# Performance work log

Hardware: AMD Instinct MI355X
Metric: run time of the kernel (lower is better)

Reference implementation:

```python
import jax, jax.numpy as jnp
import numpy as np
import math

B, C, L, N, HEAD, M, DEPTH = 16, 256, 64, 8192, 8, 12, 1
PI = math.pi
MODES = jnp.arange(M, dtype=jnp.float32) / M  # modes_list = i/num_basis


def conv1d(x, w, b=None):
    # 1x1 Conv1d == channel matmul. x: (B,Cin,T), w: (Cout,Cin)
    y = jnp.einsum('oc,bcn->bon', w, x)
    if b is not None:
        y = y + b[None, :, None]
    return y


def split_heads(x):
    # (B,C,T) -> (B,H,T,c)  matching view(B,head,C//head,T).permute(0,1,3,2)
    b, c, t = x.shape
    return x.reshape(b, HEAD, c // HEAD, t).transpose(0, 1, 3, 2)


def merge_heads(x):
    # (B,H,T,c) -> (B,C,T)
    b, h, t, c = x.shape
    return x.transpose(0, 1, 3, 2).reshape(b, h * c, t)


def self_attn(q, k, v):
    # NOTE: source multiplies by dim**0.5 (not 1/sqrt(dim)); keep faithful.
    dim = q.shape[-1]
    a = jax.nn.softmax(jnp.einsum('bhlc,bhsc->bhls', q, k) * (dim ** 0.5), axis=-1)
    return jnp.einsum('bhls,bhsc->bhlc', a, v)


def encoder(x, enc_w, enc_b, weights):
    b, c, l = x.shape
    qkv = conv1d(x, enc_w, enc_b).reshape(b, 3, c, l)
    q = split_heads(qkv[:, 0])
    k = split_heads(qkv[:, 1])
    v = split_heads(qkv[:, 2])
    attn = merge_heads(self_attn(q, k, v))  # (B,C,L)
    # Fourier basis: cat(sin, cos) over num_basis modes -> (B,C,L,2M)
    ph = MODES[None, None, None, :] * attn[..., None] * PI
    basis = jnp.concatenate([jnp.sin(ph), jnp.cos(ph)], axis=-1)
    return jnp.einsum('bclm,cm->bcl', basis, weights) + x


def decoder(x, attn, dec_w, dec_b):
    kv = split_heads(attn)                      # (B,H,L,c) latent keys/values
    q = split_heads(conv1d(x, dec_w, dec_b))    # (B,H,N,c) point queries
    return merge_heads(self_attn(q, kv, kv)) + x


def bn_lrelu(x, g, b):
    # eval-mode BatchNorm1d (running_mean=0, running_var=1, eps=1e-5) + LeakyReLU(0.2)
    y = g[None, :, None] * x / jnp.sqrt(1.0 + 1e-5) + b[None, :, None]
    return jnp.where(y >= 0, y, 0.2 * y)


def setup_inputs() -> dict:
    key = jax.random.key(0)
    ks = jax.random.split(key, 8)
    return {
        'xt': jax.random.normal(ks[0], (B, C, L), jnp.float32),
        'xn': jax.random.normal(ks[1], (B, C, N), jnp.float32),
        'weights': jax.random.uniform(ks[2], (C, 2 * M), jnp.float32) / C,
        'mask_token': jax.random.normal(ks[3], (1, C, 1), jnp.float32) * 0.02,
        'enc_w': jax.random.normal(ks[4], (3 * C, C), jnp.float32) * 0.02,
        'enc_b': jnp.zeros((3 * C,), jnp.float32),
        'dec_w': jax.random.normal(ks[5], (C, C), jnp.float32) * 0.02,
        'dec_b': jnp.zeros((C,), jnp.float32),
        'fc1_w': jax.random.normal(ks[6], (C, C), jnp.float32) * 0.02,
        'fc1_g': jnp.ones((C,), jnp.float32),
        'fc1_b': jnp.zeros((C,), jnp.float32),
        'fc2_w': jax.random.normal(ks[7], (3, C), jnp.float32) * 0.02,
        'fc2_g': jnp.ones((3,), jnp.float32),
        'fc2_b': jnp.zeros((3,), jnp.float32),
    }


def reference(xt, xn, weights, mask_token, enc_w, enc_b, dec_w, dec_b,
              fc1_w, fc1_g, fc1_b, fc2_w, fc2_g, fc2_b):
    b = xt.shape[0]
    n = xn.shape[-1]
    # ratio=1.0 -> len_keep=0 -> fully masked: mask_token broadcast, under no_grad
    x_masked = jax.lax.stop_gradient(jnp.broadcast_to(mask_token, (b, C, n)))
    enc = xt
    x = x_masked
    for _ in range(DEPTH):
        enc = encoder(enc, enc_w, enc_b, weights)
        x = decoder(x, enc, dec_w, dec_b)
    xn_pre = x
    y = bn_lrelu(conv1d(xn_pre, fc1_w), fc1_g, fc1_b)
    y = bn_lrelu(conv1d(y, fc2_w), fc2_g, fc2_b)  # (B,3,N)
    return xn_pre, y.transpose(0, 2, 1)  # ((B,C,N), (B,N,3))
```

## Files before the change

kernel.cpp:

```cpp
#include <hip/hip_runtime.h>
#include <hip/hip_bf16.h>
#include <math.h>

#define B_    16
#define C_    256
#define L_    64
#define N_    8192
#define HEAD_ 8
#define HC_   32
#define M_    12

#define SQRT32F 5.656854249492380f
#define PI_F    3.14159265358979323846f
#define BN_INV  0.99999500003749969f

typedef float v4f __attribute__((ext_vector_type(4)));

__global__ __launch_bounds__(512) void enc_half(
    const float* __restrict__ xt, const float* __restrict__ enc_w,
    const float* __restrict__ enc_b, const float* __restrict__ weights,
    float* __restrict__ enc)
{
    __shared__ float Xs[C_][L_];
    __shared__ float qkv_s[96][68];
    __shared__ float P[32][68];
    __shared__ float wts[HC_][24];
    const int t    = threadIdx.x;
    const int b    = blockIdx.x >> 4;
    const int h    = (blockIdx.x >> 1) & 7;
    const int half = blockIdx.x & 1;
    const float* xtb = xt + (size_t)b * (C_ * L_);

    #pragma unroll
    for (int i = 0; i < 8; ++i) {
        int q = t + i * 512;
        int c = q >> 4, l4 = (q & 15) * 4;
        *reinterpret_cast<float4*>(&Xs[c][l4]) =
            *reinterpret_cast<const float4*>(&xtb[q * 4]);
    }
    #pragma unroll
    for (int idx = t; idx < HC_ * 24; idx += 512)
        wts[idx / 24][idx % 24] = weights[(h * HC_) * 24 + idx];
    __syncthreads();

    {
        const int kvr  = t >> 4;
        const int kvc4 = (t & 15) * 4;
        const int qr   = t >> 3;
        const int qc4  = half * 32 + (t & 7) * 4;
        const float* wk = enc_w + (size_t)(C_ + h * HC_ + kvr) * C_;
        const float* wv = enc_w + (size_t)(2 * C_ + h * HC_ + kvr) * C_;
        const float* wq = enc_w + (size_t)(h * HC_ + (qr & 31)) * C_;
        float4 acck = {}, accv = {}, accq = {};
        #pragma unroll 2
        for (int c0 = 0; c0 < C_; c0 += 4) {
            float4 xk0 = *reinterpret_cast<const float4*>(&Xs[c0 + 0][kvc4]);
            float4 xk1 = *reinterpret_cast<const float4*>(&Xs[c0 + 1][kvc4]);
            float4 xk2 = *reinterpret_cast<const float4*>(&Xs[c0 + 2][kvc4]);
            float4 xk3 = *reinterpret_cast<const float4*>(&Xs[c0 + 3][kvc4]);
            float4 wk4 = *reinterpret_cast<const float4*>(&wk[c0]);
            float4 wv4 = *reinterpret_cast<const float4*>(&wv[c0]);
            acck.x += wk4.x * xk0.x + wk4.y * xk1.x + wk4.z * xk2.x + wk4.w * xk3.x;
            acck.y += wk4.x * xk0.y + wk4.y * xk1.y + wk4.z * xk2.y + wk4.w * xk3.y;
            acck.z += wk4.x * xk0.z + wk4.y * xk1.z + wk4.z * xk2.z + wk4.w * xk3.z;
            acck.w += wk4.x * xk0.w + wk4.y * xk1.w + wk4.z * xk2.w + wk4.w * xk3.w;
            accv.x += wv4.x * xk0.x + wv4.y * xk1.x + wv4.z * xk2.x + wv4.w * xk3.x;
            accv.y += wv4.x * xk0.y + wv4.y * xk1.y + wv4.z * xk2.y + wv4.w * xk3.y;
            accv.z += wv4.x * xk0.z + wv4.y * xk1.z + wv4.z * xk2.z + wv4.w * xk3.z;
            accv.w += wv4.x * xk0.w + wv4.y * xk1.w + wv4.z * xk2.w + wv4.w * xk3.w;
            if (t < 256) {
                float4 xq0 = *reinterpret_cast<const float4*>(&Xs[c0 + 0][qc4]);
                float4 xq1 = *reinterpret_cast<const float4*>(&Xs[c0 + 1][qc4]);
                float4 xq2 = *reinterpret_cast<const float4*>(&Xs[c0 + 2][qc4]);
                float4 xq3 = *reinterpret_cast<const float4*>(&Xs[c0 + 3][qc4]);
                float4 wq4 = *reinterpret_cast<const float4*>(&wq[c0]);
                accq.x += wq4.x * xq0.x + wq4.y * xq1.x + wq4.z * xq2.x + wq4.w * xq3.x;
                accq.y += wq4.x * xq0.y + wq4.y * xq1.y + wq4.z * xq2.y + wq4.w * xq3.y;
                accq.z += wq4.x * xq0.z + wq4.y * xq1.z + wq4.z * xq2.z + wq4.w * xq3.z;
                accq.w += wq4.x * xq0.w + wq4.y * xq1.w + wq4.z * xq2.w + wq4.w * xq3.w;
            }
        }
        float bk = enc_b[C_ + h * HC_ + kvr];
        float bv = enc_b[2 * C_ + h * HC_ + kvr];
        acck.x += bk; acck.y += bk; acck.z += bk; acck.w += bk;
        accv.x += bv; accv.y += bv; accv.z += bv; accv.w += bv;
        *reinterpret_cast<float4*>(&qkv_s[32 + kvr][kvc4]) = acck;
        *reinterpret_cast<float4*>(&qkv_s[64 + kvr][kvc4]) = accv;
        if (t < 256) {
            float bq = enc_b[h * HC_ + qr];
            accq.x += bq; accq.y += bq; accq.z += bq; accq.w += bq;
            *reinterpret_cast<float4*>(&qkv_s[qr][qc4]) = accq;
        }
    }
    __syncthreads();

    {
        const int l   = t >> 4;
        const int lp0 = (t & 15) * 4;
        const int qcol = half * 32 + l;
        float4 a4 = {0.f, 0.f, 0.f, 0.f};
        #pragma unroll
        for (int cc = 0; cc < HC_; ++cc) {
            float qv_ = qkv_s[cc][qcol];
            float4 k4 = *reinterpret_cast<const float4*>(&qkv_s[32 + cc][lp0]);
            a4.x += qv_ * k4.x; a4.y += qv_ * k4.y;
            a4.z += qv_ * k4.z; a4.w += qv_ * k4.w;
        }
        a4.x *= SQRT32F; a4.y *= SQRT32F; a4.z *= SQRT32F; a4.w *= SQRT32F;
        *reinterpret_cast<float4*>(&P[l][lp0]) = a4;
    }
    __syncthreads();

    {
        int l = t >> 4, p0 = (t & 15) * 4;
        float m = -1e30f;
        #pragma unroll
        for (int j = 0; j < 4; ++j) m = fmaxf(m, P[l][p0 + j]);
        m = fmaxf(m, __shfl_xor(m, 1));
        m = fmaxf(m, __shfl_xor(m, 2));
        m = fmaxf(m, __shfl_xor(m, 4));
        m = fmaxf(m, __shfl_xor(m, 8));
        float sum = 0.f;
        #pragma unroll
        for (int j = 0; j < 4; ++j) {
            float e = __expf(P[l][p0 + j] - m);
            P[l][p0 + j] = e;
            sum += e;
        }
        sum += __shfl_xor(sum, 1);
        sum += __shfl_xor(sum, 2);
        sum += __shfl_xor(sum, 4);
        sum += __shfl_xor(sum, 8);
        float inv = 1.0f / sum;
        #pragma unroll
        for (int j = 0; j < 4; ++j) P[l][p0 + j] *= inv;
    }
    __syncthreads();

    {
        const int l0 = (t & 15) * 2;
        const int cc = t >> 4;
        float a0 = 0.f, a1 = 0.f;
        #pragma unroll
        for (int sq = 0; sq < 16; ++sq) {
            float4 p0v = *reinterpret_cast<const float4*>(&P[l0 + 0][sq * 4]);
            float4 p1v = *reinterpret_cast<const float4*>(&P[l0 + 1][sq * 4]);
            float4 v4  = *reinterpret_cast<const float4*>(&qkv_s[64 + cc][sq * 4]);
            a0 += p0v.x * v4.x + p0v.y * v4.y + p0v.z * v4.z + p0v.w * v4.w;
            a1 += p1v.x * v4.x + p1v.y * v4.y + p1v.z * v4.z + p1v.w * v4.w;
        }
        const float* wrf = wts[cc];
        const int c  = h * HC_ + cc;
        const int lg = half * 32 + l0;
        float av[2] = {a0, a1};
        float vv[2];
        #pragma unroll
        for (int i = 0; i < 2; ++i) {
            float val = Xs[c][lg + i] + wrf[M_];
            float base = av[i] * (PI_F / (float)M_);
            float s1, c1;
            __sincosf(base, &s1, &c1);
            float sm = 0.f, cm = 1.f;
            #pragma unroll
            for (int m = 1; m < M_; ++m) {
                float sp = sm * c1 + cm * s1;
                float cp = cm * c1 - sm * s1;
                sm = sp; cm = cp;
                val += wrf[m] * sm + wrf[M_ + m] * cm;
            }
            vv[i] = val;
        }
        *reinterpret_cast<float2*>(&enc[((size_t)b * C_ + c) * L_ + lg]) =
            make_float2(vv[0], vv[1]);
    }
}

__global__ __launch_bounds__(64) void dec_attn(const float* __restrict__ enc,
                                               const float* __restrict__ dec_w,
                                               const float* __restrict__ dec_b,
                                               const float* __restrict__ mt,
                                               float* __restrict__ xnp_out) {
    __shared__ float qvs[HC_];
    __shared__ float aw[L_];
    const int l = threadIdx.x;
    const int b = blockIdx.x >> 3;
    const int h = blockIdx.x & 7;
    const float* ench = enc + ((size_t)b * C_ + h * HC_) * L_;

    {
        int r = l >> 1, part = l & 1;
        const float* wr = dec_w + (size_t)(h * HC_ + r) * C_ + part * 128;
        const float* mp = mt + part * 128;
        float s = 0.f;
        #pragma unroll
        for (int j = 0; j < 32; ++j) {
            float4 w4 = *reinterpret_cast<const float4*>(&wr[j * 4]);
            float4 m4 = *reinterpret_cast<const float4*>(&mp[j * 4]);
            s += w4.x * m4.x + w4.y * m4.y + w4.z * m4.z + w4.w * m4.w;
        }
        s += __shfl_xor(s, 1);
        if (part == 0) qvs[r] = s + dec_b[h * HC_ + r];
    }
    __syncthreads();

    float s = 0.f;
    #pragma unroll
    for (int cc = 0; cc < HC_; ++cc)
        s += qvs[cc] * ench[cc * L_ + l];
    s *= SQRT32F;
    float m = s;
    #pragma unroll
    for (int off = 32; off >= 1; off >>= 1) m = fmaxf(m, __shfl_xor(m, off));
    float e = __expf(s - m);
    float sum = e;
    #pragma unroll
    for (int off = 32; off >= 1; off >>= 1) sum += __shfl_xor(sum, off);
    aw[l] = e / sum;
    __syncthreads();

    if (l < HC_) {
        const float* vrow = ench + l * L_;
        float a = 0.f;
        #pragma unroll
        for (int k4 = 0; k4 < L_; k4 += 4) {
            float4 a4 = *reinterpret_cast<const float4*>(&aw[k4]);
            float4 v4 = *reinterpret_cast<const float4*>(&vrow[k4]);
            a += a4.x * v4.x + a4.y * v4.y + a4.z * v4.z + a4.w * v4.w;
        }
        int c = h * HC_ + l;
        xnp_out[b * C_ + c] = a + mt[c];
    }
}

__global__ __launch_bounds__(256) void bcast_fc(const float* __restrict__ xnp,
                                                const float* __restrict__ fc1_w,
                                                const float* __restrict__ fc1_g,
                                                const float* __restrict__ fc1_b,
                                                const float* __restrict__ fc2_w,
                                                const float* __restrict__ fc2_g,
                                                const float* __restrict__ fc2_b,
                                                float* __restrict__ out) {
    const int t = threadIdx.x;
    const int blk = blockIdx.x;
    if (blk >= 16) {
        int rowid = blk - 16;
        float v = xnp[rowid];
        v4f V = {v, v, v, v};
        v4f* row = reinterpret_cast<v4f*>(out + (size_t)rowid * N_);
        #pragma unroll
        for (int i = 0; i < 8; ++i)
            __builtin_nontemporal_store(V, &row[t + i * 256]);
    } else {
        int b = blk;
        __shared__ float xs[C_];
        __shared__ float y1[C_];
        __shared__ float y2s[4];
        xs[t] = xnp[b * C_ + t];
        __syncthreads();
        {
            const float* wrow = fc1_w + (size_t)t * C_;
            float s = 0.f;
            #pragma unroll 8
            for (int c4 = 0; c4 < C_; c4 += 4) {
                float4 w4 = *reinterpret_cast<const float4*>(&wrow[c4]);
                float4 x4 = *reinterpret_cast<const float4*>(&xs[c4]);
                s += w4.x * x4.x + w4.y * x4.y + w4.z * x4.z + w4.w * x4.w;
            }
            float y = fc1_g[t] * s * BN_INV + fc1_b[t];
            y1[t] = (y >= 0.f) ? y : 0.2f * y;
        }
        __syncthreads();
        if (t < 3) {
            const float* wrow = fc2_w + t * C_;
            float s = 0.f;
            #pragma unroll 8
            for (int c4 = 0; c4 < C_; c4 += 4) {
                float4 w4 = *reinterpret_cast<const float4*>(&wrow[c4]);
                float4 x4 = *reinterpret_cast<const float4*>(&y1[c4]);
                s += w4.x * x4.x + w4.y * x4.y + w4.z * x4.z + w4.w * x4.w;
            }
            float y = fc2_g[t] * s * BN_INV + fc2_b[t];
            y2s[t] = (y >= 0.f) ? y : 0.2f * y;
        }
        __syncthreads();
        float v0 = y2s[0], v1 = y2s[1], v2 = y2s[2];
        v4f pat0 = {v0, v1, v2, v0};
        v4f pat1 = {v1, v2, v0, v1};
        v4f pat2 = {v2, v0, v1, v2};
        int r = t % 3;
        v4f a = (r == 0) ? pat0 : (r == 1) ? pat1 : pat2;
        v4f bb = (r == 0) ? pat1 : (r == 1) ? pat2 : pat0;
        v4f c = (r == 0) ? pat2 : (r == 1) ? pat0 : pat1;
        v4f* o1 = reinterpret_cast<v4f*>(
            out + (size_t)B_ * C_ * N_ + (size_t)b * (N_ * 3));
        #pragma unroll
        for (int i = 0; i < 24; i += 3) {
            __builtin_nontemporal_store(a,  &o1[t + (i + 0) * 256]);
            __builtin_nontemporal_store(bb, &o1[t + (i + 1) * 256]);
            __builtin_nontemporal_store(c,  &o1[t + (i + 2) * 256]);
        }
    }
}

extern "C" void kernel_launch(void* const* d_in, const int* in_sizes, int n_in,
                              void* d_out, int out_size, void* d_ws, size_t ws_size,
                              hipStream_t stream) {
    const float* xt      = (const float*)d_in[0];
    const float* weights = (const float*)d_in[2];
    const float* mt      = (const float*)d_in[3];
    const float* enc_w   = (const float*)d_in[4];
    const float* enc_b   = (const float*)d_in[5];
    const float* dec_w   = (const float*)d_in[6];
    const float* dec_b   = (const float*)d_in[7];
    const float* fc1_w   = (const float*)d_in[8];
    const float* fc1_g   = (const float*)d_in[9];
    const float* fc1_b   = (const float*)d_in[10];
    const float* fc2_w   = (const float*)d_in[11];
    const float* fc2_g   = (const float*)d_in[12];
    const float* fc2_b   = (const float*)d_in[13];

    float* ws  = (float*)d_ws;
    float* enc = ws;
    float* xnp = ws + 262144;

    float* out = (float*)d_out;

    enc_half<<<256, 512, 0, stream>>>(xt, enc_w, enc_b, weights, enc);
    dec_attn<<<128, 64, 0, stream>>>(enc, dec_w, dec_b, mt, xnp);
    bcast_fc<<<4112, 256, 0, stream>>>(xnp, fc1_w, fc1_g, fc1_b,
                                       fc2_w, fc2_g, fc2_b, out);
}
```

Measured before the change: 55.88 us.

## Fuse encoder, decoder, and broadcast kernels into one cooperative kernel

Merges the three kernels into a single cooperative launch of 256 blocks of 512 threads, separating the encoder, decoder-attention, and broadcast/FC phases with grid-wide syncs. The broadcast of 4096 rows is redistributed so that 240 blocks write 17 rows each and the first 16 blocks write one row each and also run the FC head. This removes two kernel launch gaps, at the cost of grid-barrier overhead and far fewer blocks issuing the large output stores (256 instead of 4112).

```diff
diff --git a/kernel.cpp b/kernel.cpp
--- a/kernel.cpp
+++ b/kernel.cpp
@@ -1,6 +1,9 @@
 #include <hip/hip_runtime.h>
+#include <hip/hip_cooperative_groups.h>
 #include <hip/hip_bf16.h>
 #include <math.h>
+
+namespace cg = cooperative_groups;
 
 #define B_    16
 #define C_    256
@@ -16,258 +19,268 @@
 
 typedef float v4f __attribute__((ext_vector_type(4)));
 
-__global__ __launch_bounds__(512) void enc_half(
+__global__ __launch_bounds__(512) void mega(
     const float* __restrict__ xt, const float* __restrict__ enc_w,
     const float* __restrict__ enc_b, const float* __restrict__ weights,
-    float* __restrict__ enc)
+    const float* __restrict__ dec_w, const float* __restrict__ dec_b,
+    const float* __restrict__ mt, const float* __restrict__ fc1_w,
+    const float* __restrict__ fc1_g, const float* __restrict__ fc1_b,
+    const float* __restrict__ fc2_w, const float* __restrict__ fc2_g,
+    const float* __restrict__ fc2_b, float* __restrict__ enc_g,
+    float* __restrict__ xnp_g, float* __restrict__ out)
 {
     __shared__ float Xs[C_][L_];
     __shared__ float qkv_s[96][68];
     __shared__ float P[32][68];
     __shared__ float wts[HC_][24];
-    const int t    = threadIdx.x;
-    const int b    = blockIdx.x >> 4;
-    const int h    = (blockIdx.x >> 1) & 7;
-    const int half = blockIdx.x & 1;
-    const float* xtb = xt + (size_t)b * (C_ * L_);
-
-    #pragma unroll
-    for (int i = 0; i < 8; ++i) {
-        int q = t + i * 512;
-        int c = q >> 4, l4 = (q & 15) * 4;
-        *reinterpret_cast<float4*>(&Xs[c][l4]) =
-            *reinterpret_cast<const float4*>(&xtb[q * 4]);
-    }
-    #pragma unroll
-    for (int idx = t; idx < HC_ * 24; idx += 512)
-        wts[idx / 24][idx % 24] = weights[(h * HC_) * 24 + idx];
-    __syncthreads();
-
-    {
-        const int kvr  = t >> 4;
-        const int kvc4 = (t & 15) * 4;
-        const int qr   = t >> 3;
-        const int qc4  = half * 32 + (t & 7) * 4;
-        const float* wk = enc_w + (size_t)(C_ + h * HC_ + kvr) * C_;
-        const float* wv = enc_w + (size_t)(2 * C_ + h * HC_ + kvr) * C_;
-        const float* wq = enc_w + (size_t)(h * HC_ + (qr & 31)) * C_;
-        float4 acck = {}, accv = {}, accq = {};
-        #pragma unroll 2
-        for (int c0 = 0; c0 < C_; c0 += 4) {
-            float4 xk0 = *reinterpret_cast<const float4*>(&Xs[c0 + 0][kvc4]);
-            float4 xk1 = *reinterpret_cast<const float4*>(&Xs[c0 + 1][kvc4]);
-            float4 xk2 = *reinterpret_cast<const float4*>(&Xs[c0 + 2][kvc4]);
-            float4 xk3 = *reinterpret_cast<const float4*>(&Xs[c0 + 3][kvc4]);
-            float4 wk4 = *reinterpret_cast<const float4*>(&wk[c0]);
-            float4 wv4 = *reinterpret_cast<const float4*>(&wv[c0]);
-            acck.x += wk4.x * xk0.x + wk4.y * xk1.x + wk4.z * xk2.x + wk4.w * xk3.x;
-            acck.y += wk4.x * xk0.y + wk4.y * xk1.y + wk4.z * xk2.y + wk4.w * xk3.y;
-            acck.z += wk4.x * xk0.z + wk4.y * xk1.z + wk4.z * xk2.z + wk4.w * xk3.z;
-            acck.w += wk4.x * xk0.w + wk4.y * xk1.w + wk4.z * xk2.w + wk4.w * xk3.w;
-            accv.x += wv4.x * xk0.x + wv4.y * xk1.x + wv4.z * xk2.x + wv4.w * xk3.x;
-            accv.y += wv4.x * xk0.y + wv4.y * xk1.y + wv4.z * xk2.y + wv4.w * xk3.y;
-            accv.z += wv4.x * xk0.z + wv4.y * xk1.z + wv4.z * xk2.z + wv4.w * xk3.z;
-            accv.w += wv4.x * xk0.w + wv4.y * xk1.w + wv4.z * xk2.w + wv4.w * xk3.w;
-            if (t < 256) {
-                float4 xq0 = *reinterpret_cast<const float4*>(&Xs[c0 + 0][qc4]);
-                float4 xq1 = *reinterpret_cast<const float4*>(&Xs[c0 + 1][qc4]);
-                float4 xq2 = *reinterpret_cast<const float4*>(&Xs[c0 + 2][qc4]);
-                float4 xq3 = *reinterpret_cast<const float4*>(&Xs[c0 + 3][qc4]);
-                float4 wq4 = *reinterpret_cast<const float4*>(&wq[c0]);
-                accq.x += wq4.x * xq0.x + wq4.y * xq1.x + wq4.z * xq2.x + wq4.w * xq3.x;
-                accq.y += wq4.x * xq0.y + wq4.y * xq1.y + wq4.z * xq2.y + wq4.w * xq3.y;
-                accq.z += wq4.x * xq0.z + wq4.y * xq1.z + wq4.z * xq2.z + wq4.w * xq3.z;
-                accq.w += wq4.x * xq0.w + wq4.y * xq1.w + wq4.z * xq2.w + wq4.w * xq3.w;
-            }
-        }
-        float bk = enc_b[C_ + h * HC_ + kvr];
-        float bv = enc_b[2 * C_ + h * HC_ + kvr];
-        acck.x += bk; acck.y += bk; acck.z += bk; acck.w += bk;
-        accv.x += bv; accv.y += bv; accv.z += bv; accv.w += bv;
-        *reinterpret_cast<float4*>(&qkv_s[32 + kvr][kvc4]) = acck;
-        *reinterpret_cast<float4*>(&qkv_s[64 + kvr][kvc4]) = accv;
-        if (t < 256) {
-            float bq = enc_b[h * HC_ + qr];
-            accq.x += bq; accq.y += bq; accq.z += bq; accq.w += bq;
-            *reinterpret_cast<float4*>(&qkv_s[qr][qc4]) = accq;
-        }
-    }
-    __syncthreads();
-
-    {
-        const int l   = t >> 4;
-        const int lp0 = (t & 15) * 4;
-        const int qcol = half * 32 + l;
-        float4 a4 = {0.f, 0.f, 0.f, 0.f};
-        #pragma unroll
-        for (int cc = 0; cc < HC_; ++cc) {
-            float qv_ = qkv_s[cc][qcol];
-            float4 k4 = *reinterpret_cast<const float4*>(&qkv_s[32 + cc][lp0]);
-            a4.x += qv_ * k4.x; a4.y += qv_ * k4.y;
-            a4.z += qv_ * k4.z; a4.w += qv_ * k4.w;
-        }
-        a4.x *= SQRT32F; a4.y *= SQRT32F; a4.z *= SQRT32F; a4.w *= SQRT32F;
-        *reinterpret_cast<float4*>(&P[l][lp0]) = a4;
-    }
-    __syncthreads();
-
-    {
-        int l = t >> 4, p0 = (t & 15) * 4;
-        float m = -1e30f;
-        #pragma unroll
-        for (int j = 0; j < 4; ++j) m = fmaxf(m, P[l][p0 + j]);
-        m = fmaxf(m, __shfl_xor(m, 1));
-        m = fmaxf(m, __shfl_xor(m, 2));
-        m = fmaxf(m, __shfl_xor(m, 4));
-        m = fmaxf(m, __shfl_xor(m, 8));
-        float sum = 0.f;
-        #pragma unroll
-        for (int j = 0; j < 4; ++j) {
-            float e = __expf(P[l][p0 + j] - m);
-            P[l][p0 + j] = e;
-            sum += e;
-        }
-        sum += __shfl_xor(sum, 1);
-        sum += __shfl_xor(sum, 2);
-        sum += __shfl_xor(sum, 4);
-        sum += __shfl_xor(sum, 8);
-        float inv = 1.0f / sum;
-        #pragma unroll
-        for (int j = 0; j < 4; ++j) P[l][p0 + j] *= inv;
-    }
-    __syncthreads();
-
-    {
-        const int l0 = (t & 15) * 2;
-        const int cc = t >> 4;
-        float a0 = 0.f, a1 = 0.f;
-        #pragma unroll
-        for (int sq = 0; sq < 16; ++sq) {
-            float4 p0v = *reinterpret_cast<const float4*>(&P[l0 + 0][sq * 4]);
-            float4 p1v = *reinterpret_cast<const float4*>(&P[l0 + 1][sq * 4]);
-            float4 v4  = *reinterpret_cast<const float4*>(&qkv_s[64 + cc][sq * 4]);
-            a0 += p0v.x * v4.x + p0v.y * v4.y + p0v.z * v4.z + p0v.w * v4.w;
-            a1 += p1v.x * v4.x + p1v.y * v4.y + p1v.z * v4.z + p1v.w * v4.w;
-        }
-        const float* wrf = wts[cc];
-        const int c  = h * HC_ + cc;
-        const int lg = half * 32 + l0;
-        float av[2] = {a0, a1};
-        float vv[2];
-        #pragma unroll
-        for (int i = 0; i < 2; ++i) {
-            float val = Xs[c][lg + i] + wrf[M_];
-            float base = av[i] * (PI_F / (float)M_);
-            float s1, c1;
-            __sincosf(base, &s1, &c1);
-            float sm = 0.f, cm = 1.f;
-            #pragma unroll
-            for (int m = 1; m < M_; ++m) {
-                float sp = sm * c1 + cm * s1;
-                float cp = cm * c1 - sm * s1;
-                sm = sp; cm = cp;
-                val += wrf[m] * sm + wrf[M_ + m] * cm;
-            }
-            vv[i] = val;
-        }
-        *reinterpret_cast<float2*>(&enc[((size_t)b * C_ + c) * L_ + lg]) =
-            make_float2(vv[0], vv[1]);
-    }
-}
-
-__global__ __launch_bounds__(64) void dec_attn(const float* __restrict__ enc,
-                                               const float* __restrict__ dec_w,
-                                               const float* __restrict__ dec_b,
-                                               const float* __restrict__ mt,
-                                               float* __restrict__ xnp_out) {
     __shared__ float qvs[HC_];
     __shared__ float aw[L_];
-    const int l = threadIdx.x;
-    const int b = blockIdx.x >> 3;
-    const int h = blockIdx.x & 7;
-    const float* ench = enc + ((size_t)b * C_ + h * HC_) * L_;
+    __shared__ float fcb[2][C_];
+    __shared__ float y2s[4];
+    const int t   = threadIdx.x;
+    const int bid = blockIdx.x;
 
     {
-        int r = l >> 1, part = l & 1;
-        const float* wr = dec_w + (size_t)(h * HC_ + r) * C_ + part * 128;
-        const float* mp = mt + part * 128;
-        float s = 0.f;
+        const int b    = bid >> 4;
+        const int h    = (bid >> 1) & 7;
+        const int half = bid & 1;
+        const float* xtb = xt + (size_t)b * (C_ * L_);
+
         #pragma unroll
-        for (int j = 0; j < 32; ++j) {
-            float4 w4 = *reinterpret_cast<const float4*>(&wr[j * 4]);
-            float4 m4 = *reinterpret_cast<const float4*>(&mp[j * 4]);
-            s += w4.x * m4.x + w4.y * m4.y + w4.z * m4.z + w4.w * m4.w;
-        }
-        s += __shfl_xor(s, 1);
-        if (part == 0) qvs[r] = s + dec_b[h * HC_ + r];
+        for (int i = 0; i < 8; ++i) {
+            int q = t + i * 512;
+            int c = q >> 4, l4 = (q & 15) * 4;
+            *reinterpret_cast<float4*>(&Xs[c][l4]) =
+                *reinterpret_cast<const float4*>(&xtb[q * 4]);
+        }
+        #pragma unroll
+        for (int idx = t; idx < HC_ * 24; idx += 512)
+            wts[idx / 24][idx % 24] = weights[(h * HC_) * 24 + idx];
+        __syncthreads();
+
+        {
+            const int kvr  = t >> 4;
+            const int kvc4 = (t & 15) * 4;
+            const int qr   = t >> 3;
+            const int qc4  = half * 32 + (t & 7) * 4;
+            const float* wk = enc_w + (size_t)(C_ + h * HC_ + kvr) * C_;
+            const float* wv = enc_w + (size_t)(2 * C_ + h * HC_ + kvr) * C_;
+            const float* wq = enc_w + (size_t)(h * HC_ + (qr & 31)) * C_;
+            float4 acck = {}, accv = {}, accq = {};
+            #pragma unroll 2
+            for (int c0 = 0; c0 < C_; c0 += 4) {
+                float4 xk0 = *reinterpret_cast<const float4*>(&Xs[c0 + 0][kvc4]);
+                float4 xk1 = *reinterpret_cast<const float4*>(&Xs[c0 + 1][kvc4]);
+                float4 xk2 = *reinterpret_cast<const float4*>(&Xs[c0 + 2][kvc4]);
+                float4 xk3 = *reinterpret_cast<const float4*>(&Xs[c0 + 3][kvc4]);
+                float4 wk4 = *reinterpret_cast<const float4*>(&wk[c0]);
+                float4 wv4 = *reinterpret_cast<const float4*>(&wv[c0]);
+                acck.x += wk4.x * xk0.x + wk4.y * xk1.x + wk4.z * xk2.x + wk4.w * xk3.x;
+                acck.y += wk4.x * xk0.y + wk4.y * xk1.y + wk4.z * xk2.y + wk4.w * xk3.y;
+                acck.z += wk4.x * xk0.z + wk4.y * xk1.z + wk4.z * xk2.z + wk4.w * xk3.z;
+                acck.w += wk4.x * xk0.w + wk4.y * xk1.w + wk4.z * xk2.w + wk4.w * xk3.w;
+                accv.x += wv4.x * xk0.x + wv4.y * xk1.x + wv4.z * xk2.x + wv4.w * xk3.x;
+                accv.y += wv4.x * xk0.y + wv4.y * xk1.y + wv4.z * xk2.y + wv4.w * xk3.y;
+                accv.z += wv4.x * xk0.z + wv4.y * xk1.z + wv4.z * xk2.z + wv4.w * xk3.z;
+                accv.w += wv4.x * xk0.w + wv4.y * xk1.w + wv4.z * xk2.w + wv4.w * xk3.w;
+                if (t < 256) {
+                    float4 xq0 = *reinterpret_cast<const float4*>(&Xs[c0 + 0][qc4]);
+                    float4 xq1 = *reinterpret_cast<const float4*>(&Xs[c0 + 1][qc4]);
+                    float4 xq2 = *reinterpret_cast<const float4*>(&Xs[c0 + 2][qc4]);
+                    float4 xq3 = *reinterpret_cast<const float4*>(&Xs[c0 + 3][qc4]);
+                    float4 wq4 = *reinterpret_cast<const float4*>(&wq[c0]);
+                    accq.x += wq4.x * xq0.x + wq4.y * xq1.x + wq4.z * xq2.x + wq4.w * xq3.x;
+                    accq.y += wq4.x * xq0.y + wq4.y * xq1.y + wq4.z * xq2.y + wq4.w * xq3.y;
+                    accq.z += wq4.x * xq0.z + wq4.y * xq1.z + wq4.z * xq2.z + wq4.w * xq3.z;
+                    accq.w += wq4.x * xq0.w + wq4.y * xq1.w + wq4.z * xq2.w + wq4.w * xq3.w;
+                }
+            }
+            float bk = enc_b[C_ + h * HC_ + kvr];
+            float bv = enc_b[2 * C_ + h * HC_ + kvr];
+            acck.x += bk; acck.y += bk; acck.z += bk; acck.w += bk;
+            accv.x += bv; accv.y += bv; accv.z += bv; accv.w += bv;
+            *reinterpret_cast<float4*>(&qkv_s[32 + kvr][kvc4]) = acck;
+            *reinterpret_cast<float4*>(&qkv_s[64 + kvr][kvc4]) = accv;
+            if (t < 256) {
+                float bq = enc_b[h * HC_ + qr];
+                accq.x += bq; accq.y += bq; accq.z += bq; accq.w += bq;
+                *reinterpret_cast<float4*>(&qkv_s[qr][qc4]) = accq;
+            }
+        }
+        __syncthreads();
+
+        {
+            const int l = t >> 4;
+            const int lp0 = (t & 15) * 4;
+            const int qcol = half * 32 + l;
+            float4 a4 = {0.f, 0.f, 0.f, 0.f};
+            #pragma unroll
+            for (int cc = 0; cc < HC_; ++cc) {
+                float qv_ = qkv_s[cc][qcol];
+                float4 k4 = *reinterpret_cast<const float4*>(&qkv_s[32 + cc][lp0]);
+                a4.x += qv_ * k4.x; a4.y += qv_ * k4.y;
+                a4.z += qv_ * k4.z; a4.w += qv_ * k4.w;
+            }
+            a4.x *= SQRT32F; a4.y *= SQRT32F; a4.z *= SQRT32F; a4.w *= SQRT32F;
+            *reinterpret_cast<float4*>(&P[l][lp0]) = a4;
+        }
+        __syncthreads();
+
+        {
+            int l = t >> 4, p0 = (t & 15) * 4;
+            float m = -1e30f;
+            #pragma unroll
+            for (int j = 0; j < 4; ++j) m = fmaxf(m, P[l][p0 + j]);
+            m = fmaxf(m, __shfl_xor(m, 1));
+            m = fmaxf(m, __shfl_xor(m, 2));
+            m = fmaxf(m, __shfl_xor(m, 4));
+            m = fmaxf(m, __shfl_xor(m, 8));
+            float sum = 0.f;
+            #pragma unroll
+            for (int j = 0; j < 4; ++j) {
+                float e = __expf(P[l][p0 + j] - m);
+                P[l][p0 + j] = e;
+                sum += e;
+            }
+            sum += __shfl_xor(sum, 1);
+            sum += __shfl_xor(sum, 2);
+            sum += __shfl_xor(sum, 4);
+            sum += __shfl_xor(sum, 8);
+            float inv = 1.0f / sum;
+            #pragma unroll
+            for (int j = 0; j < 4; ++j) P[l][p0 + j] *= inv;
+        }
+        __syncthreads();
+
+        {
+            const int l0 = (t & 15) * 2;
+            const int cc = t >> 4;
+            float a0 = 0.f, a1 = 0.f;
+            #pragma unroll
+            for (int sq = 0; sq < 16; ++sq) {
+                float4 p0v = *reinterpret_cast<const float4*>(&P[l0 + 0][sq * 4]);
+                float4 p1v = *reinterpret_cast<const float4*>(&P[l0 + 1][sq * 4]);
+                float4 v4  = *reinterpret_cast<const float4*>(&qkv_s[64 + cc][sq * 4]);
+                a0 += p0v.x * v4.x + p0v.y * v4.y + p0v.z * v4.z + p0v.w * v4.w;
+                a1 += p1v.x * v4.x + p1v.y * v4.y + p1v.z * v4.z + p1v.w * v4.w;
+            }
+            const float* wrf = wts[cc];
+            const int c  = h * HC_ + cc;
+            const int lg = half * 32 + l0;
+            float av[2] = {a0, a1};
+            float vv[2];
+            #pragma unroll
+            for (int i = 0; i < 2; ++i) {
+                float val = Xs[c][lg + i] + wrf[M_];
+                float base = av[i] * (PI_F / (float)M_);
+                float s1, c1;
+                __sincosf(base, &s1, &c1);
+                float sm = 0.f, cm = 1.f;
+                #pragma unroll
+                for (int m = 1; m < M_; ++m) {
+                    float sp = sm * c1 + cm * s1;
+                    float cp = cm * c1 - sm * s1;
+                    sm = sp; cm = cp;
+                    val += wrf[m] * sm + wrf[M_ + m] * cm;
+                }
+                vv[i] = val;
+            }
+            *reinterpret_cast<float2*>(&enc_g[((size_t)b * C_ + c) * L_ + lg]) =
+                make_float2(vv[0], vv[1]);
+        }
     }
-    __syncthreads();
-
-    float s = 0.f;
-    #pragma unroll
-    for (int cc = 0; cc < HC_; ++cc)
-        s += qvs[cc] * ench[cc * L_ + l];
-    s *= SQRT32F;
-    float m = s;
-    #pragma unroll
-    for (int off = 32; off >= 1; off >>= 1) m = fmaxf(m, __shfl_xor(m, off));
-    float e = __expf(s - m);
-    float sum = e;
-    #pragma unroll
-    for (int off = 32; off >= 1; off >>= 1) sum += __shfl_xor(sum, off);
-    aw[l] = e / sum;
-    __syncthreads();
-
-    if (l < HC_) {
-        const float* vrow = ench + l * L_;
-        float a = 0.f;
+
+    cg::this_grid().sync();
+
+    if (bid < 128) {
+        const int b = bid >> 3;
+        const int h = bid & 7;
+        const float* ench = enc_g + ((size_t)b * C_ + h * HC_) * L_;
+
+        if (t < 64) {
+            int r = t >> 1, part = t & 1;
+            const float* wr = dec_w + (size_t)(h * HC_ + r) * C_ + part * 128;
+            const float* mp = mt + part * 128;
+            float s = 0.f;
+            #pragma unroll
+            for (int j = 0; j < 32; ++j) {
+                float4 w4 = *reinterpret_cast<const float4*>(&wr[j * 4]);
+                float4 m4 = *reinterpret_cast<const float4*>(&mp[j * 4]);
+                s += w4.x * m4.x + w4.y * m4.y + w4.z * m4.z + w4.w * m4.w;
+            }
+            s += __shfl_xor(s, 1);
+            if (part == 0) qvs[r] = s + dec_b[h * HC_ + r];
+        }
+        __syncthreads();
+        if (t < 64) {
+            int l = t;
+            float s = 0.f;
+            #pragma unroll
+            for (int cc = 0; cc < HC_; ++cc)
+                s += qvs[cc] * ench[cc * L_ + l];
+            s *= SQRT32F;
+            float m = s;
+            #pragma unroll
+            for (int off = 32; off >= 1; off >>= 1) m = fmaxf(m, __shfl_xor(m, off));
+            float e = __expf(s - m);
+            float sum = e;
+            #pragma unroll
+            for (int off = 32; off >= 1; off >>= 1) sum += __shfl_xor(sum, off);
+            aw[l] = e / sum;
+        }
+        __syncthreads();
+        if (t < HC_) {
+            const float* vrow = ench + t * L_;
+            float a = 0.f;
+            #pragma unroll
+            for (int k4 = 0; k4 < L_; k4 += 4) {
+                float4 a4 = *reinterpret_cast<const float4*>(&aw[k4]);
+                float4 v4 = *reinterpret_cast<const float4*>(&vrow[k4]);
+                a += a4.x * v4.x + a4.y * v4.y + a4.z * v4.z + a4.w * v4.w;
+            }
+            int c = h * HC_ + t;
+            xnp_g[b * C_ + c] = a + mt[c];
+        }
+    }
+
+    cg::this_grid().sync();
+
+    if (bid >= 16) {
+        int r0 = (bid - 16) * 17;
         #pragma unroll
-        for (int k4 = 0; k4 < L_; k4 += 4) {
-            float4 a4 = *reinterpret_cast<const float4*>(&aw[k4]);
-            float4 v4 = *reinterpret_cast<const float4*>(&vrow[k4]);
-            a += a4.x * v4.x + a4.y * v4.y + a4.z * v4.z + a4.w * v4.w;
-        }
-        int c = h * HC_ + l;
-        xnp_out[b * C_ + c] = a + mt[c];
-    }
-}
-
-__global__ __launch_bounds__(256) void bcast_fc(const float* __restrict__ xnp,
-                                                const float* __restrict__ fc1_w,
-                                                const float* __restrict__ fc1_g,
-                                                const float* __restrict__ fc1_b,
-                                                const float* __restrict__ fc2_w,
-                                                const float* __restrict__ fc2_g,
-                                                const float* __restrict__ fc2_b,
-                                                float* __restrict__ out) {
-    const int t = threadIdx.x;
-    const int blk = blockIdx.x;
-    if (blk >= 16) {
-        int rowid = blk - 16;
-        float v = xnp[rowid];
-        v4f V = {v, v, v, v};
-        v4f* row = reinterpret_cast<v4f*>(out + (size_t)rowid * N_);
-        #pragma unroll
-        for (int i = 0; i < 8; ++i)
-            __builtin_nontemporal_store(V, &row[t + i * 256]);
+        for (int i = 0; i < 17; ++i) {
+            int row = r0 + i;
+            float v = xnp_g[row];
+            v4f V = {v, v, v, v};
+            v4f* rp = reinterpret_cast<v4f*>(out + (size_t)row * N_);
+            #pragma unroll
+            for (int j = 0; j < 4; ++j)
+                __builtin_nontemporal_store(V, &rp[t + j * 512]);
+        }
     } else {
-        int b = blk;
-        __shared__ float xs[C_];
-        __shared__ float y1[C_];
-        __shared__ float y2s[4];
-        xs[t] = xnp[b * C_ + t];
-        __syncthreads();
-        {
+        {
+            int row = 4080 + bid;
+            float v = xnp_g[row];
+            v4f V = {v, v, v, v};
+            v4f* rp = reinterpret_cast<v4f*>(out + (size_t)row * N_);
+            #pragma unroll
+            for (int j = 0; j < 4; ++j)
+                __builtin_nontemporal_store(V, &rp[t + j * 512]);
+        }
+        const int b = bid;
+        if (t < C_) fcb[0][t] = xnp_g[b * C_ + t];
+        __syncthreads();
+        if (t < C_) {
             const float* wrow = fc1_w + (size_t)t * C_;
             float s = 0.f;
             #pragma unroll 8
             for (int c4 = 0; c4 < C_; c4 += 4) {
                 float4 w4 = *reinterpret_cast<const float4*>(&wrow[c4]);
-                float4 x4 = *reinterpret_cast<const float4*>(&xs[c4]);
+                float4 x4 = *reinterpret_cast<const float4*>(&fcb[0][c4]);
                 s += w4.x * x4.x + w4.y * x4.y + w4.z * x4.z + w4.w * x4.w;
             }
             float y = fc1_g[t] * s * BN_INV + fc1_b[t];
-            y1[t] = (y >= 0.f) ? y : 0.2f * y;
+            fcb[1][t] = (y >= 0.f) ? y : 0.2f * y;
         }
         __syncthreads();
         if (t < 3) {
@@ -276,7 +289,7 @@
             #pragma unroll 8
             for (int c4 = 0; c4 < C_; c4 += 4) {
                 float4 w4 = *reinterpret_cast<const float4*>(&wrow[c4]);
-                float4 x4 = *reinterpret_cast<const float4*>(&y1[c4]);
+                float4 x4 = *reinterpret_cast<const float4*>(&fcb[1][c4]);
                 s += w4.x * x4.x + w4.y * x4.y + w4.z * x4.z + w4.w * x4.w;
             }
             float y = fc2_g[t] * s * BN_INV + fc2_b[t];
@@ -288,16 +301,16 @@
         v4f pat1 = {v1, v2, v0, v1};
         v4f pat2 = {v2, v0, v1, v2};
         int r = t % 3;
-        v4f a = (r == 0) ? pat0 : (r == 1) ? pat1 : pat2;
-        v4f bb = (r == 0) ? pat1 : (r == 1) ? pat2 : pat0;
-        v4f c = (r == 0) ? pat2 : (r == 1) ? pat0 : pat1;
+        v4f pA = (r == 0) ? pat0 : (r == 1) ? pat1 : pat2;
+        v4f pB = (r == 0) ? pat2 : (r == 1) ? pat0 : pat1;
+        v4f pC = (r == 0) ? pat1 : (r == 1) ? pat2 : pat0;
         v4f* o1 = reinterpret_cast<v4f*>(
             out + (size_t)B_ * C_ * N_ + (size_t)b * (N_ * 3));
         #pragma unroll
-        for (int i = 0; i < 24; i += 3) {
-            __builtin_nontemporal_store(a,  &o1[t + (i + 0) * 256]);
-            __builtin_nontemporal_store(bb, &o1[t + (i + 1) * 256]);
-            __builtin_nontemporal_store(c,  &o1[t + (i + 2) * 256]);
+        for (int i = 0; i < 12; i += 3) {
+            __builtin_nontemporal_store(pA, &o1[t + (i + 0) * 512]);
+            __builtin_nontemporal_store(pB, &o1[t + (i + 1) * 512]);
+            __builtin_nontemporal_store(pC, &o1[t + (i + 2) * 512]);
         }
     }
 }
@@ -319,14 +332,17 @@
     const float* fc2_g   = (const float*)d_in[12];
     const float* fc2_b   = (const float*)d_in[13];
 
-    float* ws  = (float*)d_ws;
-    float* enc = ws;
-    float* xnp = ws + 262144;
-
-    float* out = (float*)d_out;
-
-    enc_half<<<256, 512, 0, stream>>>(xt, enc_w, enc_b, weights, enc);
-    dec_attn<<<128, 64, 0, stream>>>(enc, dec_w, dec_b, mt, xnp);
-    bcast_fc<<<4112, 256, 0, stream>>>(xnp, fc1_w, fc1_g, fc1_b,
-                                       fc2_w, fc2_g, fc2_b, out);
+    float* ws    = (float*)d_ws;
+    float* enc_g = ws;
+    float* xnp_g = ws + 262144;
+    float* out   = (float*)d_out;
+
+    void* args[] = {
+        (void*)&xt, (void*)&enc_w, (void*)&enc_b, (void*)&weights,
+        (void*)&dec_w, (void*)&dec_b, (void*)&mt, (void*)&fc1_w,
+        (void*)&fc1_g, (void*)&fc1_b, (void*)&fc2_w, (void*)&fc2_g,
+        (void*)&fc2_b, (void*)&enc_g, (void*)&xnp_g, (void*)&out
+    };
+    hipLaunchCooperativeKernel((void*)mega, dim3(256), dim3(512),
+                               args, 0, stream);
 }
```

After: 114.2 us. +104.4%, slower.
